# Kernel tuning notes

Measured on AMD Instinct MI355X. Metric: run time of the kernel, lower is better.

## Reference

```python
import jax, jax.numpy as jnp
import numpy as np


def setup_inputs() -> dict:
    key = jax.random.key(0)
    k1, k2 = jax.random.split(key)
    B, H, W, D = 4096, 64, 64, 512
    inputs = jax.random.normal(k1, (B, D), dtype=jnp.float32)
    # keras 'random_uniform' initializer default range [-0.05, 0.05]
    weights_map = jax.random.uniform(k2, (H, W, D), dtype=jnp.float32,
                                     minval=-0.05, maxval=0.05)
    return {"inputs": inputs, "weights_map": weights_map}


def reference(inputs, weights_map):
    # inputs: (B, D); weights_map: (H, W, D)
    H, W, D = weights_map.shape
    flat_w = weights_map.reshape(-1, D)              # (N, D), N = H*W
    # avoids materializing the (B, N, D) difference tensor)
    x_sq = jnp.sum(inputs * inputs, axis=1, keepdims=True)    # (B, 1)
    w_sq = jnp.sum(flat_w * flat_w, axis=1)                   # (N,)
    sq_dist = x_sq - 2.0 * (inputs @ flat_w.T) + w_sq         # (B, N)
    sq_dist = jnp.maximum(sq_dist, 0.0)
    bmu_flat = jnp.argmin(sq_dist, axis=1)                    # (B,)
    bmu_y = (bmu_flat // W).astype(jnp.int32)
    bmu_x = (bmu_flat % W).astype(jnp.int32)
    bmu_indices = jnp.stack([bmu_y, bmu_x], axis=1)           # (B, 2)
    min_sq = jnp.take_along_axis(sq_dist, bmu_flat[:, None], axis=1)[:, 0]
    quantization_errors = jnp.sqrt(min_sq)                    # (B,)
    return bmu_indices, quantization_errors
```

## Files before the change

### kernel.cpp

```cpp
#include <hip/hip_runtime.h>

#define B_ROWS 4096
#define N_COLS 4096
#define DIM    512
#define LDK    1024

typedef __attribute__((ext_vector_type(8))) short short8;
typedef __attribute__((ext_vector_type(4))) float floatx4;

__device__ __forceinline__ unsigned short f2bf_rn(float f) {
    unsigned u = __float_as_uint(f);
    u += 0x7fffu + ((u >> 16) & 1u);
    return (unsigned short)(u >> 16);
}
__device__ __forceinline__ float bf2f(unsigned short h) {
    return __uint_as_float(((unsigned)h) << 16);
}

__device__ __forceinline__ unsigned long long pack_key(float v, int idx) {
    unsigned u = __float_as_uint(v);
    u = (u & 0x80000000u) ? ~u : (u | 0x80000000u);
    return ((unsigned long long)u << 32) | (unsigned)idx;
}

__device__ __forceinline__ void async16(const unsigned short* g, unsigned short* l) {
    __builtin_amdgcn_global_load_lds(
        (__attribute__((address_space(1))) void*)g,
        (__attribute__((address_space(3))) void*)l, 16, 0, 0);
}

__global__ __launch_bounds__(256) void som_convert(
    const float* __restrict__ X, const float* __restrict__ Wt,
    unsigned short* __restrict__ Xc, unsigned short* __restrict__ Wc,
    float* __restrict__ x_sq, float* __restrict__ w_sq,
    unsigned long long* __restrict__ packed)
{
    int wave = threadIdx.x >> 6, lane = threadIdx.x & 63;
    int grow = blockIdx.x * 4 + wave;
    bool isX = grow < B_ROWS;
    const float* src = isX ? (X + (size_t)grow * DIM)
                           : (Wt + (size_t)(grow - B_ROWS) * DIM);
    const float4* p4 = (const float4*)src;
    float4 a = p4[lane * 2], b = p4[lane * 2 + 1];
    float f[8] = {a.x, a.y, a.z, a.w, b.x, b.y, b.z, b.w};
    short8 hi, lo;
    float s = 0.f;
    #pragma unroll
    for (int t = 0; t < 8; ++t) {
        unsigned short h = f2bf_rn(f[t]);
        hi[t] = (short)h;
        lo[t] = (short)f2bf_rn(f[t] - bf2f(h));
        s = fmaf(f[t], f[t], s);
    }
    unsigned short* dst = (isX ? Xc + (size_t)grow * LDK
                               : Wc + (size_t)(grow - B_ROWS) * LDK) + lane * 8;
    *(short8*)(dst)       = hi;
    *(short8*)(dst + 512) = lo;
    #pragma unroll
    for (int off = 32; off >= 1; off >>= 1) s += __shfl_xor(s, off, 64);
    if (lane == 0) {
        if (isX) { x_sq[grow] = s; packed[grow] = ~0ull; }
        else     { w_sq[grow - B_ROWS] = s; }
    }
}

__global__ __launch_bounds__(256, 3) void som_dist_v6(
    const unsigned short* __restrict__ Xc, const unsigned short* __restrict__ Wc,
    const float* __restrict__ w_sq, unsigned long long* __restrict__ packed)
{
    __shared__ __align__(16) unsigned short L[16384];
    const int tid  = threadIdx.x;
    const int wave = tid >> 6, lane = tid & 63;
    const int quad = lane >> 4, t16 = lane & 15;
    const int wr = wave >> 1, wc = wave & 1;

    const int bid = blockIdx.y * 32 + blockIdx.x;
    const int xcd = bid & 7, wix = bid >> 3;
    const int bm = (xcd >> 2) * 16 + (wix & 15);
    const int bn = (xcd & 3) * 8 + (wix >> 4);

    const int sg = wave & 1;
    const bool stB = (wave >= 2);
    const unsigned short* gsrc =
        (stB ? Wc + (size_t)bn * 128 * LDK : Xc + (size_t)bm * 128 * LDK)
        + (size_t)(sg * 64 + t16) * LDK + quad * 8;
    unsigned short* const lhi = &L[(stB ? 8192 : 0) + sg * 2048];
    unsigned short* const llo = lhi + 4096;

    const unsigned short* const pA = &L[wr * 2048 + lane * 8];
    const unsigned short* const pB = &L[8192 + wc * 2048 + lane * 8];

    floatx4 acc[4][4];
    #pragma unroll
    for (int i = 0; i < 4; ++i)
        #pragma unroll
        for (int j = 0; j < 4; ++j) acc[i][j] = (floatx4){0.f, 0.f, 0.f, 0.f};

    #pragma unroll 1
    for (int k0 = 0; k0 < DIM; k0 += 32) {
        __syncthreads();
        #pragma unroll
        for (int q = 0; q < 4; ++q) {
            async16(gsrc + k0 + q * 16 * LDK,       lhi + q * 512);
            async16(gsrc + k0 + q * 16 * LDK + 512, llo + q * 512);
        }
        __syncthreads();

        short8 ah[4], bh[4], x[4];
        #pragma unroll
        for (int i = 0; i < 4; ++i) ah[i] = *(const short8*)(pA + i * 512);
        #pragma unroll
        for (int j = 0; j < 4; ++j) bh[j] = *(const short8*)(pB + j * 512);
        #pragma unroll
        for (int i = 0; i < 4; ++i)
            #pragma unroll
            for (int j = 0; j < 4; ++j)
                acc[i][j] = __builtin_amdgcn_mfma_f32_16x16x32_bf16(
                    ah[i], bh[j], acc[i][j], 0, 0, 0);

        #pragma unroll
        for (int j = 0; j < 4; ++j) x[j] = *(const short8*)(pB + j * 512 + 4096);
        #pragma unroll
        for (int i = 0; i < 4; ++i)
            #pragma unroll
            for (int j = 0; j < 4; ++j)
                acc[i][j] = __builtin_amdgcn_mfma_f32_16x16x32_bf16(
                    ah[i], x[j], acc[i][j], 0, 0, 0);

        #pragma unroll
        for (int i = 0; i < 4; ++i) x[i] = *(const short8*)(pA + i * 512 + 4096);
        #pragma unroll
        for (int i = 0; i < 4; ++i)
            #pragma unroll
            for (int j = 0; j < 4; ++j)
                acc[i][j] = __builtin_amdgcn_mfma_f32_16x16x32_bf16(
                    x[i], bh[j], acc[i][j], 0, 0, 0);
    }

    const int col0 = bn * 128 + wc * 64 + t16;
    float wq[4];
    #pragma unroll
    for (int j = 0; j < 4; ++j) wq[j] = w_sq[col0 + j * 16];
    const int row_base = bm * 128 + wr * 64 + quad * 4;
    #pragma unroll
    for (int i = 0; i < 4; ++i) {
        #pragma unroll
        for (int r = 0; r < 4; ++r) {
            unsigned long long best = ~0ull;
            #pragma unroll
            for (int j = 0; j < 4; ++j) {
                float val = fmaf(-2.f, acc[i][j][r], wq[j]);
                unsigned long long key = pack_key(val, col0 + j * 16);
                best = (key < best) ? key : best;
            }
            #pragma unroll
            for (int m = 1; m <= 8; m <<= 1) {
                unsigned long long o = __shfl_xor(best, m, 64);
                best = (o < best) ? o : best;
            }
            if (t16 == 0)
                atomicMin(&packed[row_base + i * 16 + r], best);
        }
    }
}

__global__ __launch_bounds__(256) void som_finalize(
    const unsigned long long* __restrict__ packed,
    const float* __restrict__ x_sq, float* __restrict__ out)
{
    int b = blockIdx.x * 256 + threadIdx.x;
    unsigned long long p = packed[b];
    unsigned idx = (unsigned)(p & 0xffffffffull);
    unsigned key = (unsigned)(p >> 32);
    unsigned u = (key & 0x80000000u) ? (key & 0x7fffffffu) : ~key;
    float val = __uint_as_float(u);
    float sq = fmaxf(x_sq[b] + val, 0.f);
    out[2 * b]     = (float)(idx >> 6);
    out[2 * b + 1] = (float)(idx & 63);
    out[2 * B_ROWS + b] = sqrtf(sq);
}

extern "C" void kernel_launch(void* const* d_in, const int* in_sizes, int n_in,
                              void* d_out, int out_size, void* d_ws, size_t ws_size,
                              hipStream_t stream) {
    const float* X  = (const float*)d_in[0];
    const float* Wt = (const float*)d_in[1];
    float* out = (float*)d_out;

    unsigned long long* packed = (unsigned long long*)d_ws;
    float* x_sq = (float*)((char*)d_ws + (32 << 10));
    float* w_sq = (float*)((char*)d_ws + (48 << 10));
    unsigned short* Xc = (unsigned short*)((char*)d_ws + (64 << 10));
    unsigned short* Wc = (unsigned short*)((char*)d_ws + (64 << 10) + ((size_t)B_ROWS * LDK * 2));

    som_convert<<<dim3((B_ROWS + N_COLS) / 4), dim3(256), 0, stream>>>(
        X, Wt, Xc, Wc, x_sq, w_sq, packed);
    som_dist_v6<<<dim3(32, 32), dim3(256), 0, stream>>>(
        Xc, Wc, w_sq, packed);
    som_finalize<<<dim3(B_ROWS / 256), dim3(256), 0, stream>>>(packed, x_sq, out);
}
```

Baseline: 137.9 us.

## Pre-swizzle bf16 hi/lo operands into MFMA fragment layout and load directly from global

The convert kernel now writes the bf16 hi/lo split of X and W in a layout that matches MFMA fragment order, tiled by 16 rows. The distance kernel then drops shared memory and its two barriers per k-step and loads fragments straight from global into registers. It also removes the XCD-aware block remapping and raises the occupancy hint to 4 blocks per CU. Without LDS, fragment reuse across waves in a block depends on L1/L2 caching. Each wave issues more global loads, and the lack of explicit prefetching could expose memory latency.

```diff
diff --git a/kernel.cpp b/kernel.cpp
--- a/kernel.cpp
+++ b/kernel.cpp
@@ -3,7 +3,6 @@
 #define B_ROWS 4096
 #define N_COLS 4096
 #define DIM    512
-#define LDK    1024
 
 typedef __attribute__((ext_vector_type(8))) short short8;
 typedef __attribute__((ext_vector_type(4))) float floatx4;
@@ -23,11 +22,6 @@
     return ((unsigned long long)u << 32) | (unsigned)idx;
 }
 
-__device__ __forceinline__ void async16(const unsigned short* g, unsigned short* l) {
-    __builtin_amdgcn_global_load_lds(
-        (__attribute__((address_space(1))) void*)g,
-        (__attribute__((address_space(3))) void*)l, 16, 0, 0);
-}
 
 __global__ __launch_bounds__(256) void som_convert(
     const float* __restrict__ X, const float* __restrict__ Wt,
@@ -38,8 +32,9 @@
     int wave = threadIdx.x >> 6, lane = threadIdx.x & 63;
     int grow = blockIdx.x * 4 + wave;
     bool isX = grow < B_ROWS;
-    const float* src = isX ? (X + (size_t)grow * DIM)
-                           : (Wt + (size_t)(grow - B_ROWS) * DIM);
+    int local = isX ? grow : grow - B_ROWS;
+    const float* src = isX ? (X + (size_t)local * DIM)
+                           : (Wt + (size_t)local * DIM);
     const float4* p4 = (const float4*)src;
     float4 a = p4[lane * 2], b = p4[lane * 2 + 1];
     float f[8] = {a.x, a.y, a.z, a.w, b.x, b.y, b.z, b.w};
@@ -52,43 +47,32 @@
         lo[t] = (short)f2bf_rn(f[t] - bf2f(h));
         s = fmaf(f[t], f[t], s);
     }
-    unsigned short* dst = (isX ? Xc + (size_t)grow * LDK
-                               : Wc + (size_t)(grow - B_ROWS) * LDK) + lane * 8;
-    *(short8*)(dst)       = hi;
-    *(short8*)(dst + 512) = lo;
+    int R = local >> 4, rr = local & 15;
+    size_t off = ((size_t)R * 16 + (lane >> 2)) * 1024
+               + (size_t)(rr + 16 * (lane & 3)) * 8;
+    unsigned short* arr = isX ? Xc : Wc;
+    *(short8*)(arr + off)       = hi;
+    *(short8*)(arr + off + 512) = lo;
     #pragma unroll
-    for (int off = 32; off >= 1; off >>= 1) s += __shfl_xor(s, off, 64);
+    for (int off2 = 32; off2 >= 1; off2 >>= 1) s += __shfl_xor(s, off2, 64);
     if (lane == 0) {
         if (isX) { x_sq[grow] = s; packed[grow] = ~0ull; }
-        else     { w_sq[grow - B_ROWS] = s; }
+        else     { w_sq[local] = s; }
     }
 }
 
-__global__ __launch_bounds__(256, 3) void som_dist_v6(
+__global__ __launch_bounds__(256, 4) void som_dist_v9(
     const unsigned short* __restrict__ Xc, const unsigned short* __restrict__ Wc,
     const float* __restrict__ w_sq, unsigned long long* __restrict__ packed)
 {
-    __shared__ __align__(16) unsigned short L[16384];
     const int tid  = threadIdx.x;
     const int wave = tid >> 6, lane = tid & 63;
     const int quad = lane >> 4, t16 = lane & 15;
     const int wr = wave >> 1, wc = wave & 1;
+    const int bm = blockIdx.y, bn = blockIdx.x;
 
-    const int bid = blockIdx.y * 32 + blockIdx.x;
-    const int xcd = bid & 7, wix = bid >> 3;
-    const int bm = (xcd >> 2) * 16 + (wix & 15);
-    const int bn = (xcd & 3) * 8 + (wix >> 4);
-
-    const int sg = wave & 1;
-    const bool stB = (wave >= 2);
-    const unsigned short* gsrc =
-        (stB ? Wc + (size_t)bn * 128 * LDK : Xc + (size_t)bm * 128 * LDK)
-        + (size_t)(sg * 64 + t16) * LDK + quad * 8;
-    unsigned short* const lhi = &L[(stB ? 8192 : 0) + sg * 2048];
-    unsigned short* const llo = lhi + 4096;
-
-    const unsigned short* const pA = &L[wr * 2048 + lane * 8];
-    const unsigned short* const pB = &L[8192 + wc * 2048 + lane * 8];
+    const unsigned short* Abase = Xc + (size_t)(bm * 8 + wr * 4) * 16384 + lane * 8;
+    const unsigned short* Bbase = Wc + (size_t)(bn * 8 + wc * 4) * 16384 + lane * 8;
 
     floatx4 acc[4][4];
     #pragma unroll
@@ -96,45 +80,38 @@
         #pragma unroll
         for (int j = 0; j < 4; ++j) acc[i][j] = (floatx4){0.f, 0.f, 0.f, 0.f};
 
-    #pragma unroll 1
-    for (int k0 = 0; k0 < DIM; k0 += 32) {
-        __syncthreads();
+    #pragma unroll 2
+    for (int kt = 0; kt < 16; ++kt) {
+        const unsigned short* ak = Abase + kt * 1024;
+        const unsigned short* bk = Bbase + kt * 1024;
+        short8 ah[4], bh[4], bl[4], al[4];
         #pragma unroll
-        for (int q = 0; q < 4; ++q) {
-            async16(gsrc + k0 + q * 16 * LDK,       lhi + q * 512);
-            async16(gsrc + k0 + q * 16 * LDK + 512, llo + q * 512);
-        }
-        __syncthreads();
+        for (int i = 0; i < 4; ++i) ah[i] = *(const short8*)(ak + i * 16384);
+        #pragma unroll
+        for (int j = 0; j < 4; ++j) bh[j] = *(const short8*)(bk + j * 16384);
+        #pragma unroll
+        for (int j = 0; j < 4; ++j) bl[j] = *(const short8*)(bk + j * 16384 + 512);
+        #pragma unroll
+        for (int i = 0; i < 4; ++i) al[i] = *(const short8*)(ak + i * 16384 + 512);
 
-        short8 ah[4], bh[4], x[4];
-        #pragma unroll
-        for (int i = 0; i < 4; ++i) ah[i] = *(const short8*)(pA + i * 512);
-        #pragma unroll
-        for (int j = 0; j < 4; ++j) bh[j] = *(const short8*)(pB + j * 512);
         #pragma unroll
         for (int i = 0; i < 4; ++i)
             #pragma unroll
             for (int j = 0; j < 4; ++j)
                 acc[i][j] = __builtin_amdgcn_mfma_f32_16x16x32_bf16(
                     ah[i], bh[j], acc[i][j], 0, 0, 0);
-
-        #pragma unroll
-        for (int j = 0; j < 4; ++j) x[j] = *(const short8*)(pB + j * 512 + 4096);
         #pragma unroll
         for (int i = 0; i < 4; ++i)
             #pragma unroll
             for (int j = 0; j < 4; ++j)
                 acc[i][j] = __builtin_amdgcn_mfma_f32_16x16x32_bf16(
-                    ah[i], x[j], acc[i][j], 0, 0, 0);
-
-        #pragma unroll
-        for (int i = 0; i < 4; ++i) x[i] = *(const short8*)(pA + i * 512 + 4096);
+                    ah[i], bl[j], acc[i][j], 0, 0, 0);
         #pragma unroll
         for (int i = 0; i < 4; ++i)
             #pragma unroll
             for (int j = 0; j < 4; ++j)
                 acc[i][j] = __builtin_amdgcn_mfma_f32_16x16x32_bf16(
-                    x[i], bh[j], acc[i][j], 0, 0, 0);
+                    al[i], bh[j], acc[i][j], 0, 0, 0);
     }
 
     const int col0 = bn * 128 + wc * 64 + t16;
@@ -191,11 +168,11 @@
     float* x_sq = (float*)((char*)d_ws + (32 << 10));
     float* w_sq = (float*)((char*)d_ws + (48 << 10));
     unsigned short* Xc = (unsigned short*)((char*)d_ws + (64 << 10));
-    unsigned short* Wc = (unsigned short*)((char*)d_ws + (64 << 10) + ((size_t)B_ROWS * LDK * 2));
+    unsigned short* Wc = (unsigned short*)((char*)d_ws + (64 << 10) + ((size_t)B_ROWS * DIM * 2 * 2));
 
     som_convert<<<dim3((B_ROWS + N_COLS) / 4), dim3(256), 0, stream>>>(
         X, Wt, Xc, Wc, x_sq, w_sq, packed);
-    som_dist_v6<<<dim3(32, 32), dim3(256), 0, stream>>>(
+    som_dist_v9<<<dim3(N_COLS / 128, B_ROWS / 128), dim3(256), 0, stream>>>(
         Xc, Wc, w_sq, packed);
     som_finalize<<<dim3(B_ROWS / 256), dim3(256), 0, stream>>>(packed, x_sq, out);
 }
```

After: 132.0 us. 4.3% less time.
